# Optimization experiments

Measured on AMD Instinct MI355X. Metric: run time of the kernel, lower is better.

Reference implementation:

```python
import jax, jax.numpy as jnp
import numpy as np

PRE_NMS_TOPN = 6000   # cfg.TEST.RPN_PRE_NMS_TOP_N
POST_NMS_TOPN = 1000  # cfg.TEST.RPN_POST_NMS_TOP_N
NMS_THRESH = 0.7      # cfg.TEST.RPN_NMS_THRESH
MIN_SIZE = 0.0        # cfg.TEST.RPN_MIN_SIZE
BBOX_XFORM_CLIP = float(np.log(1000.0 / 16.0))
FEAT_STRIDE = 8.0     # 1 / spatial_scale


def _generate_anchors(base_size=16, ratios=(0.5, 1.0, 2.0), scales=(2, 4, 8, 16, 32)):
    """Standard Detectron anchor generation -> (A, 4) = (15, 4)."""
    def whctrs(a):
        w = a[2] - a[0] + 1.0
        h = a[3] - a[1] + 1.0
        return w, h, a[0] + 0.5 * (w - 1.0), a[1] + 0.5 * (h - 1.0)

    def mk(ws, hs, xc, yc):
        ws = ws[:, None]; hs = hs[:, None]
        return np.hstack([xc - 0.5 * (ws - 1.0), yc - 0.5 * (hs - 1.0),
                          xc + 0.5 * (ws - 1.0), yc + 0.5 * (hs - 1.0)])

    base = np.array([0.0, 0.0, base_size - 1.0, base_size - 1.0])
    w, h, xc, yc = whctrs(base)
    rs = np.array(ratios)
    ws = np.round(np.sqrt(w * h / rs))
    hs = np.round(ws * rs)
    ratio_anchors = mk(ws, hs, xc, yc)
    out = []
    for a in ratio_anchors:
        w, h, xc, yc = whctrs(a)
        sc = np.array(scales, dtype=np.float64)
        out.append(mk(w * sc, h * sc, xc, yc))
    return np.vstack(out).astype(np.float32)


def _proposals_one_image(all_anchors, im_info, bbox_deltas, scores):
    # bbox_deltas: (4A, H, W), scores: (A, H, W)
    deltas = bbox_deltas.transpose(1, 2, 0).reshape(-1, 4)  # (K*A, 4)
    s = scores.transpose(1, 2, 0).reshape(-1)               # (K*A,)

    # pre-NMS top-k by objectness (argpartition+argsort in original)
    top_s, order = jax.lax.top_k(s, PRE_NMS_TOPN)
    d = deltas[order]
    anc = all_anchors[order]

    # bbox_transform with weights (1,1,1,1) and dw/dh clipping
    ws = anc[:, 2] - anc[:, 0] + 1.0
    hs = anc[:, 3] - anc[:, 1] + 1.0
    cx = anc[:, 0] + 0.5 * ws
    cy = anc[:, 1] + 0.5 * hs
    dx, dy = d[:, 0], d[:, 1]
    dw = jnp.minimum(d[:, 2], BBOX_XFORM_CLIP)
    dh = jnp.minimum(d[:, 3], BBOX_XFORM_CLIP)
    pcx = dx * ws + cx
    pcy = dy * hs + cy
    pw = jnp.exp(dw) * ws
    ph = jnp.exp(dh) * hs
    x1 = pcx - 0.5 * pw
    y1 = pcy - 0.5 * ph
    x2 = pcx + 0.5 * pw - 1.0
    y2 = pcy + 0.5 * ph - 1.0

    # clip_tiled_boxes to image extent
    h_im, w_im, scale = im_info[0], im_info[1], im_info[2]
    x1 = jnp.clip(x1, 0.0, w_im - 1.0)
    y1 = jnp.clip(y1, 0.0, h_im - 1.0)
    x2 = jnp.clip(x2, 0.0, w_im - 1.0)
    y2 = jnp.clip(y2, 0.0, h_im - 1.0)
    boxes = jnp.stack([x1, y1, x2, y2], axis=1)  # (PRE, 4)

    # _filter_boxes -> validity mask (replaces gather-by-keep)
    bws = x2 - x1 + 1.0
    bhs = y2 - y1 + 1.0
    min_sz = MIN_SIZE * scale
    valid = (bws >= min_sz) & (bhs >= min_sz) & ((x1 + bws / 2.0) < w_im) & ((y1 + bhs / 2.0) < h_im)

    # greedy NMS on score-sorted boxes (boxes already sorted descending)
    areas = bws * bhs
    ix1 = jnp.maximum(x1[:, None], x1[None, :])
    iy1 = jnp.maximum(y1[:, None], y1[None, :])
    ix2 = jnp.minimum(x2[:, None], x2[None, :])
    iy2 = jnp.minimum(y2[:, None], y2[None, :])
    inter = jnp.maximum(ix2 - ix1 + 1.0, 0.0) * jnp.maximum(iy2 - iy1 + 1.0, 0.0)
    iou = inter / (areas[:, None] + areas[None, :] - inter)

    later = jnp.arange(PRE_NMS_TOPN)

    def body(i, keep):
        sup = keep[i] & (iou[i] > NMS_THRESH) & (later > i)
        return keep & ~sup

    keep = jax.lax.fori_loop(0, PRE_NMS_TOPN, body, valid)

    # fixed-size output: top POST_NMS_TOPN surviving boxes, padded (score=-1, box=0)
    masked = jnp.where(keep, top_s, -1.0)
    out_s, idx = jax.lax.top_k(masked, POST_NMS_TOPN)
    pad = (out_s > -1.0).astype(boxes.dtype)
    out_b = boxes[idx] * pad[:, None]
    return out_b, out_s


def reference(rpn_cls_prob, rpn_bbox_pred, im_info, anchors):
    N, A, H, W = rpn_cls_prob.shape
    dt = rpn_bbox_pred.dtype
    shift_x = jnp.arange(W, dtype=dt) * FEAT_STRIDE
    shift_y = jnp.arange(H, dtype=dt) * FEAT_STRIDE
    # torch.meshgrid default 'ij' ordering (faithful to original)
    sx, sy = jnp.meshgrid(shift_x, shift_y, indexing='ij')  # (W, H)
    shifts = jnp.stack([sx.ravel(), sy.ravel(), sx.ravel(), sy.ravel()], axis=1)  # (K, 4)
    all_anchors = (anchors[None, :, :] + shifts[:, None, :]).reshape(-1, 4)  # (K*A, 4)

    boxes, probs = jax.vmap(_proposals_one_image, in_axes=(None, 0, 0, 0))(
        all_anchors, im_info, rpn_bbox_pred, rpn_cls_prob)
    batch_inds = jnp.broadcast_to(jnp.arange(N, dtype=boxes.dtype)[:, None, None],
                                  (N, POST_NMS_TOPN, 1))
    rois = jnp.concatenate([batch_inds, boxes], axis=-1).reshape(-1, 5)
    return rois, probs.reshape(-1)


def setup_inputs() -> dict:
    key = jax.random.key(0)
    k1, k2 = jax.random.split(key)
    N, A, H, W = 2, 15, 128, 128
    rpn_cls_prob = jax.random.uniform(k1, (N, A, H, W), dtype=jnp.float32)
    rpn_bbox_pred = jax.random.normal(k2, (N, 4 * A, H, W), dtype=jnp.float32) * 0.2
    im_info = jnp.tile(jnp.array([[1024.0, 1024.0, 1.0]], dtype=jnp.float32), (N, 1))
    anchors = jnp.asarray(_generate_anchors())
    return {"rpn_cls_prob": rpn_cls_prob, "rpn_bbox_pred": rpn_bbox_pred,
            "im_info": im_info, "anchors": anchors}
```

## Files before the change

kernel.cpp:

```cpp
#include <hip/hip_runtime.h>
#include <hip/hip_bf16.h>

#define A_NUM 15
#define HDIM 128
#define WDIM 128
#define HW (HDIM*WDIM)
#define PER_IMG (A_NUM*HW)
#define NIMG 2
#define PRE_N 6000
#define POST_N 1000
#define NBLK 94
#define NPAD (NBLK*64)
#define SORTN 8192
#define CHUNK4 4096
#define NBIN 16384
#define HPART 16
#define PROD_T 448
#define WPT 14

typedef unsigned long long ull;

#define META_OFF   0u
#define HIST_OFF   64u
#define SEL_OFF    131136u
#define BOX_OFF    262208u
#define VALIDW_OFF 550976u
#define MASK_OFF   553024u

__device__ __forceinline__ unsigned int f2ord(float f) {
    unsigned int u = __float_as_uint(f);
    return (u & 0x80000000u) ? ~u : (u | 0x80000000u);
}
__device__ __forceinline__ float ord2f(unsigned int u) {
    unsigned int s = (u & 0x80000000u) ? (u ^ 0x80000000u) : ~u;
    return __uint_as_float(s);
}
__device__ __forceinline__ ull readlane64(ull v, int l) {
    unsigned int lo = (unsigned int)__builtin_amdgcn_readlane((int)(unsigned int)v, l);
    unsigned int hi = (unsigned int)__builtin_amdgcn_readlane((int)(unsigned int)(v >> 32), l);
    return ((ull)hi << 32) | lo;
}
__device__ __forceinline__ void barrier_lds() {
    asm volatile("s_waitcnt lgkmcnt(0)" ::: "memory");
    __builtin_amdgcn_s_barrier();
    asm volatile("" ::: "memory");
}

__global__ __launch_bounds__(1024) void k_hist16(const float* __restrict__ cls,
                                                 unsigned int* __restrict__ hist) {
    __shared__ unsigned int h[NBIN];
    int img = blockIdx.y, part = blockIdx.x;
    int t = threadIdx.x;
    for (int b = t; b < NBIN; b += 1024) h[b] = 0;
    __syncthreads();
    int base = img * PER_IMG + part * (PER_IMG / HPART);
    for (int e = t; e < PER_IMG / HPART; e += 1024) {
        unsigned int u = f2ord(cls[base + e]);
        unsigned int bin = (u >> 16) - 0x8000u;
        if (bin > (NBIN - 1)) bin = NBIN - 1;
        atomicAdd(&h[bin], 1u);
    }
    __syncthreads();
    unsigned int* hp = hist + (size_t)img * NBIN;
    for (int b = t; b < NBIN; b += 1024)
        if (h[b]) atomicAdd(&hp[b], h[b]);
}

__global__ __launch_bounds__(1024) void k_scan16(const unsigned int* __restrict__ hist,
                                                 unsigned int* __restrict__ meta) {
    __shared__ unsigned int csum[1024];
    __shared__ unsigned int aux[64];
    __shared__ unsigned int binv[16];
    int img = blockIdx.x, t = threadIdx.x;
    const unsigned int* hp = hist + (size_t)img * NBIN;
    unsigned int s = 0;
    #pragma unroll
    for (int q = 0; q < 16; ++q) s += hp[t * 16 + q];
    csum[t] = s;
    __syncthreads();
    if (t < 64) {
        unsigned int x = 0;
        #pragma unroll
        for (int q = 0; q < 16; ++q) x += csum[t * 16 + q];
        aux[t] = x;
    }
    __syncthreads();
    if (t < 64) {
        unsigned int suf = 0;
        for (int q = t; q < 64; ++q) suf += aux[q];
        ull mb1 = __ballot(suf >= PRE_N);
        int sstar = 63 - __clzll(mb1);
        unsigned int sufnext = (unsigned)__shfl((int)suf, (sstar + 1) & 63);
        unsigned int cumAbove = (sstar == 63) ? 0u : sufnext;
        unsigned int sufC = 0;
        if (t < 16) {
            for (int q = sstar * 16 + t; q < sstar * 16 + 16; ++q) sufC += csum[q];
            sufC += cumAbove;
        }
        ull mb2 = __ballot((t < 16) && (sufC >= PRE_N));
        int crel = 63 - __clzll(mb2);
        int cstar = sstar * 16 + crel;
        unsigned int cumAbove2 = (crel == 15) ? cumAbove : (unsigned)__shfl((int)sufC, crel + 1);
        if (t < 16) binv[t] = hp[cstar * 16 + t];
        unsigned int sufB = 0;
        if (t < 16) {
            for (int q = t; q < 16; ++q) sufB += binv[q];
            sufB += cumAbove2;
        }
        ull mb3 = __ballot((t < 16) && (sufB >= PRE_N));
        int brel = 63 - __clzll(mb3);
        if (t == 0) {
            meta[2 + img] = (unsigned)(cstar * 16 + brel) + 0x8000u;
            meta[img] = 0u;
        }
    }
}

__global__ __launch_bounds__(256) void k_gather(const float* __restrict__ cls,
                                                unsigned int* __restrict__ meta,
                                                ull* __restrict__ selkeys) {
    __shared__ unsigned int lcnt[NIMG], lbase[NIMG];
    int t = threadIdx.x;
    int tid = blockIdx.x * 256 + t;
    if (t < NIMG) lcnt[t] = 0;
    __syncthreads();
    unsigned int T0 = meta[2], T1 = meta[3];
    int a = tid / HW;
    int pos = tid - a * HW;
    int m = pos * A_NUM + a;
    int lane = t & 63;
    unsigned int uv[NIMG];
    bool pr[NIMG];
    unsigned int lofs[NIMG];
    #pragma unroll
    for (int img = 0; img < NIMG; ++img) {
        unsigned int T = img ? T1 : T0;
        unsigned int u = f2ord(cls[img * PER_IMG + tid]);
        uv[img] = u;
        bool pred = (u >> 16) >= T;
        pr[img] = pred;
        ull mball = __ballot((int)pred);
        unsigned int o = 0;
        if (pred) {
            int leader = __ffsll((long long)mball) - 1;
            unsigned int wbase = 0;
            if (lane == leader) wbase = atomicAdd(&lcnt[img], (unsigned)__popcll(mball));
            wbase = (unsigned)__shfl((int)wbase, leader);
            o = wbase + (unsigned)__popcll(mball & ((1ull << lane) - 1ull));
        }
        lofs[img] = o;
    }
    __syncthreads();
    if (t < NIMG) lbase[t] = atomicAdd(&meta[t], lcnt[t]);
    __syncthreads();
    #pragma unroll
    for (int img = 0; img < NIMG; ++img) {
        if (pr[img]) {
            unsigned int p = lbase[img] + lofs[img];
            if (p < SORTN)
                selkeys[(size_t)img * SORTN + p] =
                    ((ull)(~uv[img]) << 32) | (unsigned int)m;
        }
    }
}

__global__ __launch_bounds__(512) void k_sortA(ull* __restrict__ selkeys,
                                               const unsigned int* __restrict__ meta) {
    __shared__ ull key[CHUNK4];
    int img = blockIdx.x >> 1, c = blockIdx.x & 1;
    unsigned int cnt = meta[img];
    if (cnt > SORTN) cnt = SORTN;
    ull* g = selkeys + (size_t)img * SORTN;
    int base = c * CHUNK4;
    for (int i = threadIdx.x; i < CHUNK4; i += 512)
        key[i] = (base + i < (int)cnt) ? g[base + i] : ~0ull;
    __syncthreads();
    bool desc = (c & 1);
    for (int k = 2; k <= CHUNK4; k <<= 1) {
        for (int j = k >> 1; j > 0; j >>= 1) {
            for (int p = threadIdx.x; p < CHUNK4 / 2; p += 512) {
                int i = ((p & ~(j - 1)) << 1) | (p & (j - 1));
                int x = i | j;
                bool up = (((i & k) == 0) != desc);
                ull A = key[i], B = key[x];
                if ((A > B) == up) { key[i] = B; key[x] = A; }
            }
            __syncthreads();
        }
    }
    for (int i = threadIdx.x; i < CHUNK4; i += 512) g[base + i] = key[i];
}

__global__ __launch_bounds__(512) void k_sortC(ull* __restrict__ selkeys) {
    __shared__ ull key[SORTN];
    int img = blockIdx.x;
    ull* g = selkeys + (size_t)img * SORTN;
    for (int i = threadIdx.x; i < SORTN; i += 512) key[i] = g[i];
    __syncthreads();
    for (int j = SORTN / 2; j > 0; j >>= 1) {
        for (int p = threadIdx.x; p < SORTN / 2; p += 512) {
            int i = ((p & ~(j - 1)) << 1) | (p & (j - 1));
            int x = i | j;
            ull A = key[i], B = key[x];
            if (A > B) { key[i] = B; key[x] = A; }
        }
        __syncthreads();
    }
    for (int i = threadIdx.x; i < PRE_N; i += 512) g[i] = key[i];
}

__global__ void k_decode(const ull* __restrict__ selkeys,
                         const float* __restrict__ bbox, const float* __restrict__ anchors,
                         const float* __restrict__ iminfo,
                         float* __restrict__ boxsoa, ull* __restrict__ validwArr) {
    int r = blockIdx.x * blockDim.x + threadIdx.x;
    int img = blockIdx.y;
    bool in = r < PRE_N;
    int rr = in ? r : 0;
    ull keyv = selkeys[(size_t)img * SORTN + rr];
    unsigned int m = (unsigned int)(keyv & 0xFFFFFFFFu);
    unsigned int u = ~(unsigned int)(keyv >> 32);
    float score = ord2f(u);
    int q = m / A_NUM;
    int a = m - q * A_NUM;
    int w = q & (WDIM - 1);
    int h = q >> 7;
    float sx = (float)h * 8.0f;
    float sy = (float)w * 8.0f;
    float a0 = __fadd_rn(anchors[a * 4 + 0], sx);
    float a1 = __fadd_rn(anchors[a * 4 + 1], sy);
    float a2 = __fadd_rn(anchors[a * 4 + 2], sx);
    float a3 = __fadd_rn(anchors[a * 4 + 3], sy);
    float ws = __fadd_rn(__fsub_rn(a2, a0), 1.0f);
    float hs = __fadd_rn(__fsub_rn(a3, a1), 1.0f);
    float cx = __fadd_rn(a0, __fmul_rn(0.5f, ws));
    float cy = __fadd_rn(a1, __fmul_rn(0.5f, hs));
    const float* bb = bbox + (size_t)img * 4 * A_NUM * HW;
    int base = h * WDIM + w;
    float dx = bb[(a * 4 + 0) * HW + base];
    float dy = bb[(a * 4 + 1) * HW + base];
    float dwv = bb[(a * 4 + 2) * HW + base];
    float dhv = bb[(a * 4 + 3) * HW + base];
    const float CLIPV = 4.135166556742356f;
    float dw = fminf(dwv, CLIPV);
    float dh = fminf(dhv, CLIPV);
    float pcx = __fadd_rn(__fmul_rn(dx, ws), cx);
    float pcy = __fadd_rn(__fmul_rn(dy, hs), cy);
    float pw = __fmul_rn(expf(dw), ws);
    float ph = __fmul_rn(expf(dh), hs);
    float x1 = __fsub_rn(pcx, __fmul_rn(0.5f, pw));
    float y1 = __fsub_rn(pcy, __fmul_rn(0.5f, ph));
    float x2 = __fsub_rn(__fadd_rn(pcx, __fmul_rn(0.5f, pw)), 1.0f);
    float y2 = __fsub_rn(__fadd_rn(pcy, __fmul_rn(0.5f, ph)), 1.0f);
    float him = iminfo[img * 3 + 0], wim = iminfo[img * 3 + 1], scale = iminfo[img * 3 + 2];
    float wmax = __fsub_rn(wim, 1.0f), hmax = __fsub_rn(him, 1.0f);
    x1 = fminf(fmaxf(x1, 0.0f), wmax);
    y1 = fminf(fmaxf(y1, 0.0f), hmax);
    x2 = fminf(fmaxf(x2, 0.0f), wmax);
    y2 = fminf(fmaxf(y2, 0.0f), hmax);
    float bws = __fadd_rn(__fsub_rn(x2, x1), 1.0f);
    float bhs = __fadd_rn(__fsub_rn(y2, y1), 1.0f);
    float minsz = __fmul_rn(0.0f, scale);
    bool valid = (bws >= minsz) && (bhs >= minsz) &&
                 (__fadd_rn(x1, __fdiv_rn(bws, 2.0f)) < wim) &&
                 (__fadd_rn(y1, __fdiv_rn(bhs, 2.0f)) < him);
    float area = __fmul_rn(bws, bhs);
    if (in) {
        boxsoa[(0 * NIMG + img) * NPAD + r] = x1;
        boxsoa[(1 * NIMG + img) * NPAD + r] = y1;
        boxsoa[(2 * NIMG + img) * NPAD + r] = x2;
        boxsoa[(3 * NIMG + img) * NPAD + r] = y2;
        boxsoa[(4 * NIMG + img) * NPAD + r] = area;
        boxsoa[(5 * NIMG + img) * NPAD + r] = score;
    }
    ull bw = __ballot((int)(in && valid));
    if ((threadIdx.x & 63) == 0) {
        int blk = r >> 6;
        if (blk < NBLK) validwArr[img * 128 + blk] = bw;
    }
}

__global__ __launch_bounds__(256) void k_mask(const float* __restrict__ boxsoa,
                                              ull* __restrict__ Mc) {
    int cb = blockIdx.x, rbq = blockIdx.y, img = blockIdx.z;
    if ((rbq << 2) > cb) return;
    int t = threadIdx.x, wv = t >> 6, lane = t & 63;
    __shared__ float jx1[64], jy1[64], jx2[64], jy2[64], jar[64];
    const float* X1 = boxsoa + (0 * NIMG + img) * NPAD;
    const float* Y1 = boxsoa + (1 * NIMG + img) * NPAD;
    const float* X2 = boxsoa + (2 * NIMG + img) * NPAD;
    const float* Y2 = boxsoa + (3 * NIMG + img) * NPAD;
    const float* AR = boxsoa + (4 * NIMG + img) * NPAD;
    int j0 = cb * 64;
    if (t < 64) {
        int jidx = j0 + t;
        bool jin = jidx < PRE_N;
        jx1[t] = jin ? X1[jidx] : 0.0f;
        jy1[t] = jin ? Y1[jidx] : 0.0f;
        jx2[t] = jin ? X2[jidx] : 0.0f;
        jy2[t] = jin ? Y2[jidx] : 0.0f;
        jar[t] = jin ? AR[jidx] : 1.0f;
    }
    __syncthreads();
    int rb = rbq * 4 + wv;
    if (rb > cb) return;
    int r = rb * 64 + lane;
    ull bits = 0ULL;
    if (r < PRE_N) {
        float x1 = X1[r], y1 = Y1[r], x2 = X2[r], y2 = Y2[r], ai = AR[r];
        for (int jj = 0; jj < 64; ++jj) {
            int j = j0 + jj;
            if (j == r || j >= PRE_N) continue;
            float ix1 = fmaxf(x1, jx1[jj]);
            float iy1 = fmaxf(y1, jy1[jj]);
            float ix2 = fminf(x2, jx2[jj]);
            float iy2 = fminf(y2, jy2[jj]);
            float iw = fmaxf(__fadd_rn(__fsub_rn(ix2, ix1), 1.0f), 0.0f);
            float ih = fmaxf(__fadd_rn(__fsub_rn(iy2, iy1), 1.0f), 0.0f);
            float inter = __fmul_rn(iw, ih);
            float denom = __fsub_rn(__fadd_rn(ai, jar[jj]), inter);
            float iou = __fdiv_rn(inter, denom);
            if (iou > 0.7f) bits |= (1ULL << jj);
        }
    }
    Mc[((size_t)img * NBLK + cb) * NPAD + r] = bits;
}

__global__ __launch_bounds__(512, 1) void k_reduce(const ull* __restrict__ Mc,
                                                   const ull* __restrict__ validwArr,
                                                   const float* __restrict__ boxsoa,
                                                   float* __restrict__ out) {
    __shared__ ull buf[3][NPAD];
    __shared__ ull keptLDS[NBLK];
    __shared__ ull partial[2][8][64];
    __shared__ unsigned short s_list[POST_N];
    __shared__ int s_stop, s_cnt;
    int img = blockIdx.x;
    int tid = threadIdx.x;
    int wv = tid >> 6, lane = tid & 63;
    const ull* MCI = Mc + (size_t)img * NBLK * NPAD;
    ull vw_a = 0, vw_b = 0;
    ull rbufA[WPT], rbufB[WPT];
    #pragma unroll
    for (int q = 0; q < WPT; ++q) { rbufA[q] = 0ULL; rbufB[q] = 0ULL; }
    int pid = tid - 64;
    if (wv == 0) {
        vw_a = validwArr[img * 128 + lane];
        vw_b = (lane + 64 < NBLK) ? validwArr[img * 128 + lane + 64] : 0ULL;
        if (lane == 0) { s_stop = 0; s_cnt = 0; }
        partial[0][0][lane] = 0ULL;
        partial[1][0][lane] = 0ULL;
    } else {
        #pragma unroll
        for (int q = 0; q < WPT; ++q) {
            int w = pid + PROD_T * q;
            rbufA[q] = (w < 64) ? MCI[w] : 0ULL;
        }
        #pragma unroll
        for (int q = 0; q < WPT; ++q) {
            int w = pid + PROD_T * q;
            if (w < 64) buf[0][w] = rbufA[q];
        }
        #pragma unroll
        for (int q = 0; q < WPT; ++q) {
            int w = pid + PROD_T * q;
            rbufB[q] = (w < 128) ? MCI[NPAD + w] : 0ULL;
        }
        #pragma unroll
        for (int q = 0; q < WPT; ++q) {
            int w = pid + PROD_T * q;
            if (w < 128) buf[1][w] = rbufB[q];
        }
        #pragma unroll
        for (int q = 0; q < WPT; ++q) {
            int w = pid + PROD_T * q;
            rbufA[q] = (w < 192) ? MCI[2 * (size_t)NPAD + w] : 0ULL;
        }
        #pragma unroll
        for (int q = 0; q < WPT; ++q) {
            int w = pid + PROD_T * q;
            rbufB[q] = (w < 256) ? MCI[3 * (size_t)NPAD + w] : 0ULL;
        }
        partial[0][wv][lane] = 0ULL;
        partial[1][wv][lane] = 0ULL;
    }
    __syncthreads();
    int cnt = 0;
    for (int ib = 0; ib < NBLK; ++ib) {
        int bcur = ib % 3, bn1 = (ib + 1) % 3, bn2 = (ib + 2) % 3;
        if (wv == 0) {
            ull acc = 0ULL;
            if (ib > 0) {
                #pragma unroll
                for (int q = 1; q < 8; ++q) acc |= partial[ib & 1][q][lane];
                ull kwp = keptLDS[ib - 1];
                acc |= (0ULL - ((kwp >> lane) & 1ULL)) & buf[bcur][(ib - 1) * 64 + lane];
            }
            unsigned int lo = (unsigned)acc, hi = (unsigned)(acc >> 32);
            #pragma unroll
            for (int s2 = 1; s2 < 64; s2 <<= 1) {
                lo |= (unsigned)__shfl_xor((int)lo, s2);
                hi |= (unsigned)__shfl_xor((int)hi, s2);
            }
            ull sup = ((ull)hi << 32) | lo;
            ull validw = (ib < 64) ? readlane64(vw_a, ib) : readlane64(vw_b, ib - 64);
            ull d = buf[bcur][ib * 64 + lane];
            ull live = validw & ~sup;
            unsigned int dlo = (unsigned)d, dhi = (unsigned)(d >> 32);
            ull keptb = 0ULL;
            while (live) {
                int b = __ffsll((long long)live) - 1;
                keptb |= 1ULL << b;
                if (lane == 0) s_list[cnt] = (unsigned short)(ib * 64 + b);
                ++cnt;
                if (cnt >= POST_N) break;
                unsigned int rl = (unsigned)__builtin_amdgcn_readlane((int)dlo, b);
                unsigned int rh = (unsigned)__builtin_amdgcn_readlane((int)dhi, b);
                live &= ~(((ull)rh << 32) | rl);
                live &= ~(1ULL << b);
            }
            if (lane == 0) {
                keptLDS[ib] = keptb;
                s_cnt = cnt;
                if (cnt >= POST_N) s_stop = 1;
            }
        } else {
            int c_w = ib + 2;
            if (c_w < NBLK) {
                int Ww = (c_w + 1) * 64;
                if (Ww > NPAD) Ww = NPAD;
                if (ib & 1) {
                    #pragma unroll
                    for (int q = 0; q < WPT; ++q) {
                        int w = pid + PROD_T * q;
                        if (w < Ww) buf[bn2][w] = rbufB[q];
                    }
                } else {
                    #pragma unroll
                    for (int q = 0; q < WPT; ++q) {
                        int w = pid + PROD_T * q;
                        if (w < Ww) buf[bn2][w] = rbufA[q];
                    }
                }
            }
            int c_l = ib + 4;
            if (c_l < NBLK) {
                int Wn = (c_l + 1) * 64;
                if (Wn > NPAD) Wn = NPAD;
                const ull* gn = MCI + (size_t)c_l * NPAD;
                if (ib & 1) {
                    #pragma unroll
                    for (int q = 0; q < WPT; ++q) {
                        int w = pid + PROD_T * q;
                        rbufB[q] = (w < Wn) ? gn[w] : 0ULL;
                    }
                } else {
                    #pragma unroll
                    for (int q = 0; q < WPT; ++q) {
                        int w = pid + PROD_T * q;
                        rbufA[q] = (w < Wn) ? gn[w] : 0ULL;
                    }
                }
            }
            if (ib + 1 < NBLK) {
                ull part = 0ULL;
                for (int u = wv - 1; u <= ib - 1; u += 7) {
                    ull kw = keptLDS[u];
                    ull v = buf[bn1][u * 64 + lane];
                    part |= (0ULL - ((kw >> lane) & 1ULL)) & v;
                }
                partial[(ib + 1) & 1][wv][lane] = part;
            }
        }
        barrier_lds();
        if (s_stop) break;
    }
    asm volatile("s_waitcnt vmcnt(0) lgkmcnt(0)" ::: "memory");
    __syncthreads();
    int total = s_cnt > POST_N ? POST_N : s_cnt;
    for (int k = tid; k < POST_N; k += 512) {
        float x1 = 0.0f, y1 = 0.0f, x2 = 0.0f, y2 = 0.0f, sc = -1.0f;
        if (k < total) {
            int r = (int)s_list[k];
            x1 = boxsoa[(0 * NIMG + img) * NPAD + r];
            y1 = boxsoa[(1 * NIMG + img) * NPAD + r];
            x2 = boxsoa[(2 * NIMG + img) * NPAD + r];
            y2 = boxsoa[(3 * NIMG + img) * NPAD + r];
            sc = boxsoa[(5 * NIMG + img) * NPAD + r];
        }
        float* roi = out + (size_t)(img * POST_N + k) * 5;
        roi[0] = (float)img;
        roi[1] = x1;
        roi[2] = y1;
        roi[3] = x2;
        roi[4] = y2;
        out[NIMG * POST_N * 5 + img * POST_N + k] = sc;
    }
}

extern "C" void kernel_launch(void* const* d_in, const int* in_sizes, int n_in,
                              void* d_out, int out_size, void* d_ws, size_t ws_size,
                              hipStream_t stream) {
    const float* cls = (const float*)d_in[0];
    const float* bbox = (const float*)d_in[1];
    const float* iminfo = (const float*)d_in[2];
    const float* anchors = (const float*)d_in[3];
    float* out = (float*)d_out;
    char* ws = (char*)d_ws;

    unsigned int* meta = (unsigned int*)(ws + META_OFF);
    unsigned int* hist = (unsigned int*)(ws + HIST_OFF);
    ull* selkeys = (ull*)(ws + SEL_OFF);
    float* boxsoa = (float*)(ws + BOX_OFF);
    ull* validwArr = (ull*)(ws + VALIDW_OFF);
    ull* mask = (ull*)(ws + MASK_OFF);

    hipMemsetAsync(hist, 0, (size_t)NIMG * NBIN * sizeof(unsigned int), stream);
    k_hist16<<<dim3(HPART, NIMG), 1024, 0, stream>>>(cls, hist);
    k_scan16<<<NIMG, 1024, 0, stream>>>(hist, meta);
    k_gather<<<PER_IMG / 256, 256, 0, stream>>>(cls, meta, selkeys);
    k_sortA<<<2 * NIMG, 512, 0, stream>>>(selkeys, meta);
    k_sortC<<<NIMG, 512, 0, stream>>>(selkeys);
    k_decode<<<dim3((PRE_N + 255) / 256, NIMG), 256, 0, stream>>>(selkeys, bbox, anchors, iminfo,
                                                                  boxsoa, validwArr);
    k_mask<<<dim3(NBLK, (NBLK + 3) / 4, NIMG), 256, 0, stream>>>(boxsoa, mask);
    k_reduce<<<NIMG, 512, 0, stream>>>(mask, validwArr, boxsoa, out);
}
```

Measured before the change: 258.6 us.

## Shorten serial NMS critical path with transposed sub-diagonal mask and ballot-based suppression

k_mask now also computes the block just below the diagonal (row block cb+1 against column block cb) into a separate Mdm1 array. The consumer wave in k_reduce can then test suppression by the previous block's kept boxes with a per-lane AND plus one ballot, instead of a 64-lane shuffle OR reduction. Producer waves now reduce their partial suppression words to one scalar each before writing to LDS. The intra-block greedy loop switches from readlane of mask rows to per-lane alive flags and ballots. This trades extra mask work and a global load per iteration for less serial work on the single consumer wave.

```diff
diff --git a/kernel.cpp b/kernel.cpp
--- a/kernel.cpp
+++ b/kernel.cpp
@@ -25,7 +25,8 @@
 #define SEL_OFF    131136u
 #define BOX_OFF    262208u
 #define VALIDW_OFF 550976u
-#define MASK_OFF   553024u
+#define MDM1_OFF   553024u
+#define MASK_OFF   649280u
 
 __device__ __forceinline__ unsigned int f2ord(float f) {
     unsigned int u = __float_as_uint(f);
@@ -281,9 +282,10 @@
 }
 
 __global__ __launch_bounds__(256) void k_mask(const float* __restrict__ boxsoa,
-                                              ull* __restrict__ Mc) {
+                                              ull* __restrict__ Mc,
+                                              ull* __restrict__ Mdm1) {
     int cb = blockIdx.x, rbq = blockIdx.y, img = blockIdx.z;
-    if ((rbq << 2) > cb) return;
+    if ((rbq << 2) > cb + 1) return;
     int t = threadIdx.x, wv = t >> 6, lane = t & 63;
     __shared__ float jx1[64], jy1[64], jx2[64], jy2[64], jar[64];
     const float* X1 = boxsoa + (0 * NIMG + img) * NPAD;
@@ -303,7 +305,7 @@
     }
     __syncthreads();
     int rb = rbq * 4 + wv;
-    if (rb > cb) return;
+    if (rb > cb + 1 || rb >= NBLK) return;
     int r = rb * 64 + lane;
     ull bits = 0ULL;
     if (r < PRE_N) {
@@ -323,33 +325,40 @@
             if (iou > 0.7f) bits |= (1ULL << jj);
         }
     }
-    Mc[((size_t)img * NBLK + cb) * NPAD + r] = bits;
+    if (rb <= cb) Mc[((size_t)img * NBLK + cb) * NPAD + r] = bits;
+    else          Mdm1[(size_t)img * NPAD + r] = bits;
 }
 
 __global__ __launch_bounds__(512, 1) void k_reduce(const ull* __restrict__ Mc,
+                                                   const ull* __restrict__ Mdm1,
                                                    const ull* __restrict__ validwArr,
                                                    const float* __restrict__ boxsoa,
                                                    float* __restrict__ out) {
     __shared__ ull buf[3][NPAD];
     __shared__ ull keptLDS[NBLK];
-    __shared__ ull partial[2][8][64];
+    __shared__ ull partialW[2][8];
     __shared__ unsigned short s_list[POST_N];
     __shared__ int s_stop, s_cnt;
     int img = blockIdx.x;
     int tid = threadIdx.x;
     int wv = tid >> 6, lane = tid & 63;
     const ull* MCI = Mc + (size_t)img * NBLK * NPAD;
+    const ull* MD1 = Mdm1 + (size_t)img * NPAD;
     ull vw_a = 0, vw_b = 0;
     ull rbufA[WPT], rbufB[WPT];
     #pragma unroll
     for (int q = 0; q < WPT; ++q) { rbufA[q] = 0ULL; rbufB[q] = 0ULL; }
     int pid = tid - 64;
+    ull md_cur = 0ULL, keptb_prev = 0ULL;
     if (wv == 0) {
         vw_a = validwArr[img * 128 + lane];
         vw_b = (lane + 64 < NBLK) ? validwArr[img * 128 + lane + 64] : 0ULL;
-        if (lane == 0) { s_stop = 0; s_cnt = 0; }
-        partial[0][0][lane] = 0ULL;
-        partial[1][0][lane] = 0ULL;
+        if (lane == 0) {
+            s_stop = 0; s_cnt = 0;
+            partialW[0][0] = 0ULL; partialW[1][0] = 0ULL;
+            #pragma unroll
+            for (int q = 1; q < 8; ++q) { partialW[0][q] = 0ULL; partialW[1][q] = 0ULL; }
+        }
     } else {
         #pragma unroll
         for (int q = 0; q < WPT; ++q) {
@@ -381,49 +390,43 @@
             int w = pid + PROD_T * q;
             rbufB[q] = (w < 256) ? MCI[3 * (size_t)NPAD + w] : 0ULL;
         }
-        partial[0][wv][lane] = 0ULL;
-        partial[1][wv][lane] = 0ULL;
     }
     __syncthreads();
     int cnt = 0;
     for (int ib = 0; ib < NBLK; ++ib) {
         int bcur = ib % 3, bn1 = (ib + 1) % 3, bn2 = (ib + 2) % 3;
         if (wv == 0) {
-            ull acc = 0ULL;
+            ull md_nx = 0ULL;
+            if (ib + 1 < NBLK) md_nx = MD1[(ib + 1) * 64 + lane];
+            ull sup = 0ULL;
+            #pragma unroll
+            for (int q = 1; q < 8; ++q) sup |= partialW[ib & 1][q];
             if (ib > 0) {
-                #pragma unroll
-                for (int q = 1; q < 8; ++q) acc |= partial[ib & 1][q][lane];
-                ull kwp = keptLDS[ib - 1];
-                acc |= (0ULL - ((kwp >> lane) & 1ULL)) & buf[bcur][(ib - 1) * 64 + lane];
-            }
-            unsigned int lo = (unsigned)acc, hi = (unsigned)(acc >> 32);
-            #pragma unroll
-            for (int s2 = 1; s2 < 64; s2 <<= 1) {
-                lo |= (unsigned)__shfl_xor((int)lo, s2);
-                hi |= (unsigned)__shfl_xor((int)hi, s2);
-            }
-            ull sup = ((ull)hi << 32) | lo;
+                bool f = (md_cur & keptb_prev) != 0ULL;
+                sup |= __ballot((int)f);
+            }
             ull validw = (ib < 64) ? readlane64(vw_a, ib) : readlane64(vw_b, ib - 64);
             ull d = buf[bcur][ib * 64 + lane];
             ull live = validw & ~sup;
-            unsigned int dlo = (unsigned)d, dhi = (unsigned)(d >> 32);
+            bool alive = ((live >> lane) & 1ULL) != 0ULL;
             ull keptb = 0ULL;
-            while (live) {
-                int b = __ffsll((long long)live) - 1;
+            ull pending = __ballot((int)alive);
+            while (pending) {
+                int b = __ffsll((long long)pending) - 1;
                 keptb |= 1ULL << b;
                 if (lane == 0) s_list[cnt] = (unsigned short)(ib * 64 + b);
                 ++cnt;
                 if (cnt >= POST_N) break;
-                unsigned int rl = (unsigned)__builtin_amdgcn_readlane((int)dlo, b);
-                unsigned int rh = (unsigned)__builtin_amdgcn_readlane((int)dhi, b);
-                live &= ~(((ull)rh << 32) | rl);
-                live &= ~(1ULL << b);
+                if (lane > b && ((d >> b) & 1ULL)) alive = false;
+                pending = __ballot((int)alive) & ~keptb;
             }
             if (lane == 0) {
                 keptLDS[ib] = keptb;
                 s_cnt = cnt;
                 if (cnt >= POST_N) s_stop = 1;
             }
+            keptb_prev = keptb;
+            md_cur = md_nx;
         } else {
             int c_w = ib + 2;
             if (c_w < NBLK) {
@@ -469,7 +472,13 @@
                     ull v = buf[bn1][u * 64 + lane];
                     part |= (0ULL - ((kw >> lane) & 1ULL)) & v;
                 }
-                partial[(ib + 1) & 1][wv][lane] = part;
+                unsigned int lo = (unsigned)part, hi = (unsigned)(part >> 32);
+                #pragma unroll
+                for (int s2 = 1; s2 < 64; s2 <<= 1) {
+                    lo |= (unsigned)__shfl_xor((int)lo, s2);
+                    hi |= (unsigned)__shfl_xor((int)hi, s2);
+                }
+                if (lane == 0) partialW[(ib + 1) & 1][wv] = ((ull)hi << 32) | lo;
             }
         }
         barrier_lds();
@@ -513,6 +522,7 @@
     ull* selkeys = (ull*)(ws + SEL_OFF);
     float* boxsoa = (float*)(ws + BOX_OFF);
     ull* validwArr = (ull*)(ws + VALIDW_OFF);
+    ull* Mdm1 = (ull*)(ws + MDM1_OFF);
     ull* mask = (ull*)(ws + MASK_OFF);
 
     hipMemsetAsync(hist, 0, (size_t)NIMG * NBIN * sizeof(unsigned int), stream);
@@ -523,6 +533,6 @@
     k_sortC<<<NIMG, 512, 0, stream>>>(selkeys);
     k_decode<<<dim3((PRE_N + 255) / 256, NIMG), 256, 0, stream>>>(selkeys, bbox, anchors, iminfo,
                                                                   boxsoa, validwArr);
-    k_mask<<<dim3(NBLK, (NBLK + 3) / 4, NIMG), 256, 0, stream>>>(boxsoa, mask);
-    k_reduce<<<NIMG, 512, 0, stream>>>(mask, validwArr, boxsoa, out);
-}
+    k_mask<<<dim3(NBLK, (NBLK + 7) / 4, NIMG), 256, 0, stream>>>(boxsoa, mask, Mdm1);
+    k_reduce<<<NIMG, 512, 0, stream>>>(mask, Mdm1, validwArr, boxsoa, out);
+}
```

New measurement: 293.8 us. +13.6%, slower.
